# Performance work log

Measured on AMD Instinct MI355X. Metric: run time of the kernel, lower is better.

## Reference

```python
import jax, jax.numpy as jnp
import numpy as np

N_NODES = 50000
N_EDGES = 800000
D = 64
K_ORDER = 8


def setup_inputs() -> dict:
    key = jax.random.key(0)
    k1, k2, k3, k4 = jax.random.split(key, 4)
    x = jax.random.normal(k1, (N_NODES, D), dtype=jnp.float32)
    edge_index = jax.random.randint(k2, (2, N_EDGES), 0, N_NODES, dtype=jnp.int64)
    edge_weight = jax.random.uniform(k3, (N_EDGES,), dtype=jnp.float32)
    weight = jax.random.normal(k4, (K_ORDER, D, D), dtype=jnp.float32) * 0.05
    bias = jnp.zeros((D,), dtype=jnp.float32)
    return {"x": x, "edge_index": edge_index, "edge_weight": edge_weight,
            "weight": weight, "bias": bias}


def _propagate(h, src, dst, edge_weight, n_nodes):
    # sparse matvec: out[i] = sum_{e: dst_e = i} w_e * h[src_e]
    msgs = edge_weight[:, None] * h[src]          # (E, D)
    return jax.ops.segment_sum(msgs, dst, num_segments=n_nodes)


def reference(x, edge_index, edge_weight, weight, bias):
    src, dst = edge_index[0], edge_index[1]
    n = x.shape[0]
    K = weight.shape[0]
    # Chebyshev recursion: T_0 = x, T_1 = L x, T_k = 2 L T_{k-1} - T_{k-2}
    Tx_prev = x                                   # T_0
    out = jnp.einsum('nd,de->ne', Tx_prev, weight[0])
    Tx_cur = _propagate(x, src, dst, edge_weight, n)  # T_1
    if K > 1:
        out = out + jnp.einsum('nd,de->ne', Tx_cur, weight[1])
    for k in range(2, K):
        Tx_next = 2.0 * _propagate(Tx_cur, src, dst, edge_weight, n) - Tx_prev
        out = out + jnp.einsum('nd,de->ne', Tx_next, weight[k])
        Tx_prev, Tx_cur = Tx_cur, Tx_next
    return out + bias
```

## Files before the change

kernel.cpp:

```cpp
#include <hip/hip_runtime.h>
#include <hip/hip_fp16.h>

#define DD  64
#define BKT 256
#define CAP 4608
#define CHK 4096


__device__ __forceinline__ unsigned pk_bf16(float a, float b) {
    unsigned ua = __float_as_uint(a), ub = __float_as_uint(b);
    ua = (ua + 0x7fffu + ((ua >> 16) & 1u)) >> 16;
    ub = (ub + 0x7fffu + ((ub >> 16) & 1u)) & 0xffff0000u;
    return (ua & 0xffffu) | ub;
}
__device__ __forceinline__ void unpk_bf16(unsigned u, float& lo, float& hi) {
    lo = __uint_as_float(u << 16);
    hi = __uint_as_float(u & 0xffff0000u);
}


__global__ __launch_bounds__(256) void p1hist_kernel(
    const int* __restrict__ ei, int* __restrict__ bh, int E, int NB)
{
    __shared__ int lh[256];
    lh[threadIdx.x] = 0;
    __syncthreads();
    for (int e = blockIdx.x * 256 + threadIdx.x; e < E; e += gridDim.x * 256)
        atomicAdd(&lh[ei[E + e] >> 8], 1);
    __syncthreads();
    if (threadIdx.x < NB && lh[threadIdx.x])
        atomicAdd(&bh[threadIdx.x], lh[threadIdx.x]);
}

__global__ __launch_bounds__(256) void p1scan_kernel(
    const int* __restrict__ bh, int* __restrict__ bptr, int* __restrict__ bcur,
    int NB, int E)
{
    __shared__ int s[256];
    int t = threadIdx.x;
    int v = (t < NB) ? bh[t] : 0;
    s[t] = v;
    __syncthreads();
    for (int off = 1; off < 256; off <<= 1) {
        int u = (t >= off) ? s[t - off] : 0;
        __syncthreads();
        s[t] += u;
        __syncthreads();
    }
    if (t < NB) { int ex = s[t] - v; bptr[t] = ex; bcur[t] = ex; }
    if (t == 0) bptr[NB] = E;
}

__global__ __launch_bounds__(256) void p1fill_kernel(
    const int* __restrict__ ei, const float* __restrict__ ew,
    int* __restrict__ bcur, uint2* __restrict__ tmp, int E, int NB)
{
    __shared__ int lh[256], gb[256], lc[256];
    int tid = threadIdx.x;
    lh[tid] = 0;
    __syncthreads();
    int base = blockIdx.x * CHK;
#pragma unroll
    for (int j = 0; j < CHK / 256; ++j) {
        int e = base + j * 256 + tid;
        if (e < E) atomicAdd(&lh[ei[E + e] >> 8], 1);
    }
    __syncthreads();
    if (tid < NB) {
        gb[tid] = lh[tid] ? atomicAdd(&bcur[tid], lh[tid]) : 0;
        lc[tid] = 0;
    }
    __syncthreads();
#pragma unroll
    for (int j = 0; j < CHK / 256; ++j) {
        int e = base + j * 256 + tid;
        if (e < E) {
            int src = ei[e], dst = ei[E + e];
            unsigned short hw = __half_as_ushort(__float2half(ew[e]));
            unsigned rec = (unsigned)(unsigned short)src | ((unsigned)hw << 16);
            int b = dst >> 8;
            int pos = gb[b] + atomicAdd(&lc[b], 1);
            tmp[pos] = make_uint2(rec, (unsigned)(dst & 255));
        }
    }
}

__global__ __launch_bounds__(1024) void p2sort_kernel(
    const uint2* __restrict__ tmp, const int* __restrict__ bptr,
    unsigned* __restrict__ edges, int* __restrict__ row_ptr,
    int N, int E, int NB)
{
    __shared__ int lh[BKT], lx[BKT], lc[BKT];
    __shared__ unsigned lout[CAP];
    int b = blockIdx.x;
    int base = bptr[b];
    int cnt = bptr[b + 1] - base;
    if (cnt > CAP) cnt = CAP;
    int t = threadIdx.x;
    if (t < BKT) lh[t] = 0;
    __syncthreads();
    for (int i = t; i < cnt; i += 1024)
        atomicAdd(&lh[tmp[base + i].y & 255], 1);
    __syncthreads();
    if (t < BKT) { lc[t] = lh[t]; lx[t] = lh[t]; }
    __syncthreads();
    for (int off = 1; off < BKT; off <<= 1) {
        int v = 0;
        if (t < BKT && t >= off) v = lx[t - off];
        __syncthreads();
        if (t < BKT && t >= off) lx[t] += v;
        __syncthreads();
    }
    if (t < BKT) { lx[t] -= lc[t]; lc[t] = 0; }
    __syncthreads();
    for (int i = t; i < cnt; i += 1024) {
        uint2 r = tmp[base + i];
        int dl = r.y & 255;
        int pos = lx[dl] + atomicAdd(&lc[dl], 1);
        lout[pos] = r.x;
    }
    __syncthreads();
    for (int i = t; i < cnt; i += 1024) edges[base + i] = lout[i];
    if (t < BKT) {
        int d = b * BKT + t;
        if (d < N) row_ptr[d] = base + lx[t];
    }
    if (b == NB - 1 && t == 0) row_ptr[N] = E;
}

__global__ __launch_bounds__(256) void quant_kernel(
    const float4* __restrict__ src, uint4* __restrict__ dst, int n8)
{
    int i = blockIdx.x * 256 + threadIdx.x;
    if (i >= n8) return;
    float4 a = src[2 * i], b = src[2 * i + 1];
    dst[i] = make_uint4(pk_bf16(a.x, a.y), pk_bf16(a.z, a.w),
                        pk_bf16(b.x, b.y), pk_bf16(b.z, b.w));
}

__global__ __launch_bounds__(256) void prop_kernel(
    const unsigned short* __restrict__ h, const unsigned short* __restrict__ prev,
    const unsigned* __restrict__ edges, const int* __restrict__ row_ptr,
    unsigned short* __restrict__ Tnext, int N)
{
    int lane = threadIdx.x & 63;
    int wid  = (blockIdx.x * 256 + threadIdx.x) >> 6;
    int n0 = wid * 2, n1 = n0 + 1;
    if (n0 >= N) return;
    bool v1 = n1 < N;

    int g  = lane >> 3;
    int c8 = (lane & 7) << 3;

    int beg0 = row_ptr[n0];
    int end0 = row_ptr[n0 + 1];
    int beg1 = end0;
    int end1 = v1 ? row_ptr[n1 + 1] : end0;

    float4 A0 = make_float4(0.f, 0.f, 0.f, 0.f), A1 = A0;
    float4 B0 = A0, B1 = A0;

    int b0 = beg0, b1 = beg1;
    while (b0 < end0 || b1 < end1) {
        unsigned RA0 = (b0 + g     < end0) ? edges[b0 + g]     : 0u;
        unsigned RB0 = (b0 + 8 + g < end0) ? edges[b0 + 8 + g] : 0u;
        unsigned RA1 = (b1 + g     < end1) ? edges[b1 + g]     : 0u;
        unsigned RB1 = (b1 + 8 + g < end1) ? edges[b1 + 8 + g] : 0u;
        float wa0 = __half2float(__ushort_as_half((unsigned short)(RA0 >> 16)));
        float wb0 = __half2float(__ushort_as_half((unsigned short)(RB0 >> 16)));
        float wa1 = __half2float(__ushort_as_half((unsigned short)(RA1 >> 16)));
        float wb1 = __half2float(__ushort_as_half((unsigned short)(RB1 >> 16)));
        const uint4 va0 = *reinterpret_cast<const uint4*>(
            &h[(size_t)(RA0 & 0xffffu) * DD + c8]);
        const uint4 vb0 = *reinterpret_cast<const uint4*>(
            &h[(size_t)(RB0 & 0xffffu) * DD + c8]);
        const uint4 va1 = *reinterpret_cast<const uint4*>(
            &h[(size_t)(RA1 & 0xffffu) * DD + c8]);
        const uint4 vb1 = *reinterpret_cast<const uint4*>(
            &h[(size_t)(RB1 & 0xffffu) * DD + c8]);
        float lo, hi;
        unpk_bf16(va0.x, lo, hi); A0.x = fmaf(wa0, lo, A0.x); A0.y = fmaf(wa0, hi, A0.y);
        unpk_bf16(va0.y, lo, hi); A0.z = fmaf(wa0, lo, A0.z); A0.w = fmaf(wa0, hi, A0.w);
        unpk_bf16(va0.z, lo, hi); A1.x = fmaf(wa0, lo, A1.x); A1.y = fmaf(wa0, hi, A1.y);
        unpk_bf16(va0.w, lo, hi); A1.z = fmaf(wa0, lo, A1.z); A1.w = fmaf(wa0, hi, A1.w);
        unpk_bf16(vb0.x, lo, hi); A0.x = fmaf(wb0, lo, A0.x); A0.y = fmaf(wb0, hi, A0.y);
        unpk_bf16(vb0.y, lo, hi); A0.z = fmaf(wb0, lo, A0.z); A0.w = fmaf(wb0, hi, A0.w);
        unpk_bf16(vb0.z, lo, hi); A1.x = fmaf(wb0, lo, A1.x); A1.y = fmaf(wb0, hi, A1.y);
        unpk_bf16(vb0.w, lo, hi); A1.z = fmaf(wb0, lo, A1.z); A1.w = fmaf(wb0, hi, A1.w);
        unpk_bf16(va1.x, lo, hi); B0.x = fmaf(wa1, lo, B0.x); B0.y = fmaf(wa1, hi, B0.y);
        unpk_bf16(va1.y, lo, hi); B0.z = fmaf(wa1, lo, B0.z); B0.w = fmaf(wa1, hi, B0.w);
        unpk_bf16(va1.z, lo, hi); B1.x = fmaf(wa1, lo, B1.x); B1.y = fmaf(wa1, hi, B1.y);
        unpk_bf16(va1.w, lo, hi); B1.z = fmaf(wa1, lo, B1.z); B1.w = fmaf(wa1, hi, B1.w);
        unpk_bf16(vb1.x, lo, hi); B0.x = fmaf(wb1, lo, B0.x); B0.y = fmaf(wb1, hi, B0.y);
        unpk_bf16(vb1.y, lo, hi); B0.z = fmaf(wb1, lo, B0.z); B0.w = fmaf(wb1, hi, B0.w);
        unpk_bf16(vb1.z, lo, hi); B1.x = fmaf(wb1, lo, B1.x); B1.y = fmaf(wb1, hi, B1.y);
        unpk_bf16(vb1.w, lo, hi); B1.z = fmaf(wb1, lo, B1.z); B1.w = fmaf(wb1, hi, B1.w);
        b0 += 16; b1 += 16;
    }

#pragma unroll
    for (int mk = 8; mk <= 32; mk <<= 1) {
        A0.x += __shfl_xor(A0.x, mk); A0.y += __shfl_xor(A0.y, mk);
        A0.z += __shfl_xor(A0.z, mk); A0.w += __shfl_xor(A0.w, mk);
        A1.x += __shfl_xor(A1.x, mk); A1.y += __shfl_xor(A1.y, mk);
        A1.z += __shfl_xor(A1.z, mk); A1.w += __shfl_xor(A1.w, mk);
        B0.x += __shfl_xor(B0.x, mk); B0.y += __shfl_xor(B0.y, mk);
        B0.z += __shfl_xor(B0.z, mk); B0.w += __shfl_xor(B0.w, mk);
        B1.x += __shfl_xor(B1.x, mk); B1.y += __shfl_xor(B1.y, mk);
        B1.z += __shfl_xor(B1.z, mk); B1.w += __shfl_xor(B1.w, mk);
    }

    if (prev) {
        {
            const uint4 p = *reinterpret_cast<const uint4*>(&prev[(size_t)n0 * DD + c8]);
            float lo, hi;
            unpk_bf16(p.x, lo, hi); A0.x = 2.f * A0.x - lo; A0.y = 2.f * A0.y - hi;
            unpk_bf16(p.y, lo, hi); A0.z = 2.f * A0.z - lo; A0.w = 2.f * A0.w - hi;
            unpk_bf16(p.z, lo, hi); A1.x = 2.f * A1.x - lo; A1.y = 2.f * A1.y - hi;
            unpk_bf16(p.w, lo, hi); A1.z = 2.f * A1.z - lo; A1.w = 2.f * A1.w - hi;
        }
        if (v1) {
            const uint4 p = *reinterpret_cast<const uint4*>(&prev[(size_t)n1 * DD + c8]);
            float lo, hi;
            unpk_bf16(p.x, lo, hi); B0.x = 2.f * B0.x - lo; B0.y = 2.f * B0.y - hi;
            unpk_bf16(p.y, lo, hi); B0.z = 2.f * B0.z - lo; B0.w = 2.f * B0.w - hi;
            unpk_bf16(p.z, lo, hi); B1.x = 2.f * B1.x - lo; B1.y = 2.f * B1.y - hi;
            unpk_bf16(p.w, lo, hi); B1.z = 2.f * B1.z - lo; B1.w = 2.f * B1.w - hi;
        }
    }
    if (g == 0) {
        *reinterpret_cast<uint4*>(&Tnext[(size_t)n0 * DD + c8]) =
            make_uint4(pk_bf16(A0.x, A0.y), pk_bf16(A0.z, A0.w),
                       pk_bf16(A1.x, A1.y), pk_bf16(A1.z, A1.w));
        if (v1)
            *reinterpret_cast<uint4*>(&Tnext[(size_t)n1 * DD + c8]) =
                make_uint4(pk_bf16(B0.x, B0.y), pk_bf16(B0.z, B0.w),
                           pk_bf16(B1.x, B1.y), pk_bf16(B1.z, B1.w));
    }
}

__global__ __launch_bounds__(512) void mega_gemm_kernel(
    const unsigned short* __restrict__ T0, const unsigned short* __restrict__ T1,
    const unsigned short* __restrict__ T2, const unsigned short* __restrict__ T3,
    const float* __restrict__ W, const float* __restrict__ bias,
    float* __restrict__ out, int N, int nord, int init)
{
    __shared__ float Ws[DD * DD];
    __shared__ float Ts[64][68];
    const unsigned short* Tl[4] = { T0, T1, T2, T3 };

    int nb0 = blockIdx.x * 64;
    int r = threadIdx.x >> 4, c = threadIdx.x & 15;
    int r2 = r * 2, c4 = c * 4;

    float acc[2][4];
    if (init) {
        const float4 bb = *reinterpret_cast<const float4*>(&bias[c4]);
#pragma unroll
        for (int i = 0; i < 2; ++i) {
            acc[i][0] = bb.x; acc[i][1] = bb.y; acc[i][2] = bb.z; acc[i][3] = bb.w;
        }
    } else {
#pragma unroll
        for (int i = 0; i < 2; ++i)
            acc[i][0] = acc[i][1] = acc[i][2] = acc[i][3] = 0.f;
    }

    int nl = threadIdx.x & 63, q = threadIdx.x >> 6;
    for (int kc = 0; kc < nord; ++kc) {
        __syncthreads();
        for (int i = threadIdx.x; i < DD * DD; i += 512)
            Ws[i] = W[kc * DD * DD + i];
        {
            uint4 u = make_uint4(0, 0, 0, 0);
            if (nb0 + nl < N)
                u = *reinterpret_cast<const uint4*>(
                    &Tl[kc][(size_t)(nb0 + nl) * DD + q * 8]);
            float f0, f1, f2, f3, f4, f5, f6, f7;
            unpk_bf16(u.x, f0, f1); unpk_bf16(u.y, f2, f3);
            unpk_bf16(u.z, f4, f5); unpk_bf16(u.w, f6, f7);
            *reinterpret_cast<float4*>(&Ts[nl][q * 8])     = make_float4(f0, f1, f2, f3);
            *reinterpret_cast<float4*>(&Ts[nl][q * 8 + 4]) = make_float4(f4, f5, f6, f7);
        }
        __syncthreads();
#pragma unroll 8
        for (int d = 0; d < DD; ++d) {
            float a0 = Ts[r2 + 0][d], a1 = Ts[r2 + 1][d];
            float4 b = *reinterpret_cast<const float4*>(&Ws[d * DD + c4]);
            acc[0][0] = fmaf(a0, b.x, acc[0][0]); acc[0][1] = fmaf(a0, b.y, acc[0][1]);
            acc[0][2] = fmaf(a0, b.z, acc[0][2]); acc[0][3] = fmaf(a0, b.w, acc[0][3]);
            acc[1][0] = fmaf(a1, b.x, acc[1][0]); acc[1][1] = fmaf(a1, b.y, acc[1][1]);
            acc[1][2] = fmaf(a1, b.z, acc[1][2]); acc[1][3] = fmaf(a1, b.w, acc[1][3]);
        }
    }

#pragma unroll
    for (int i = 0; i < 2; ++i) {
        int n = nb0 + r2 + i;
        if (n < N) {
            float4 o = make_float4(acc[i][0], acc[i][1], acc[i][2], acc[i][3]);
            if (!init) {
                float4 p = *reinterpret_cast<const float4*>(&out[(size_t)n * DD + c4]);
                o.x += p.x; o.y += p.y; o.z += p.z; o.w += p.w;
            }
            *reinterpret_cast<float4*>(&out[(size_t)n * DD + c4]) = o;
        }
    }
}


static inline size_t rup(size_t x) { return (x + 255) & ~(size_t)255; }

extern "C" void kernel_launch(void* const* d_in, const int* in_sizes, int n_in,
                              void* d_out, int out_size, void* d_ws, size_t ws_size,
                              hipStream_t stream) {
    const float* x    = (const float*)d_in[0];
    const int*   ei   = (const int*)  d_in[1];
    const float* ew   = (const float*)d_in[2];
    const float* W    = (const float*)d_in[3];
    const float* bias = (const float*)d_in[4];
    float* out = (float*)d_out;

    int N = in_sizes[0] / DD;
    int E = in_sizes[2];
    int K = in_sizes[3] / (DD * DD);
    int NB = (N + BKT - 1) / BKT;

    size_t nb_bf = (size_t)N * DD * sizeof(unsigned short);

    char* w = (char*)d_ws;
    unsigned short* B[5];
    for (int i = 0; i < 5; ++i) { B[i] = (unsigned short*)w; w += rup(nb_bf); }
    unsigned* edges  = (unsigned*)w;  w += rup((size_t)E * sizeof(unsigned));
    int* row_ptr = (int*)w;           w += rup((size_t)(N + 1) * sizeof(int));
    int* bh      = (int*)w;           w += rup((size_t)NB * sizeof(int));
    int* bptr    = (int*)w;           w += rup((size_t)(NB + 1) * sizeof(int));
    int* bcur    = (int*)w;           w += rup((size_t)NB * sizeof(int));
    uint2* tmp   = (uint2*)B[1];

    int pb   = (N + 7) / 8;
    int gb64 = (N + 63) / 64;
    int n8   = (N * DD) / 8;
    int qb   = (n8 + 255) / 256;
    int fb   = (E + CHK - 1) / CHK;

    hipMemsetAsync(bh, 0, (size_t)NB * sizeof(int), stream);
    p1hist_kernel<<<512, 256, 0, stream>>>(ei, bh, E, NB);
    p1scan_kernel<<<1, 256, 0, stream>>>(bh, bptr, bcur, NB, E);
    p1fill_kernel<<<fb, 256, 0, stream>>>(ei, ew, bcur, tmp, E, NB);
    p2sort_kernel<<<NB, 1024, 0, stream>>>(tmp, bptr, edges, row_ptr, N, E, NB);

    quant_kernel<<<qb, 256, 0, stream>>>((const float4*)x, (uint4*)B[0], n8);

    int done = 0;
    for (int k = 1; k < K; ++k) {
        const unsigned short* cur  = B[(k - 1) % 5];
        const unsigned short* prev = (k >= 2) ? B[(k - 2) % 5] : nullptr;
        unsigned short*       nxt  = B[k % 5];
        prop_kernel<<<pb, 256, 0, stream>>>(cur, prev, edges, row_ptr, nxt, N);
        if (k % 4 == 3) {
            int c0 = done;
            mega_gemm_kernel<<<gb64, 512, 0, stream>>>(
                B[(c0 + 0) % 5], B[(c0 + 1) % 5], B[(c0 + 2) % 5], B[(c0 + 3) % 5],
                W + (size_t)c0 * DD * DD, bias, out, N, 4, done == 0);
            done += 4;
        }
    }
    if (done < K) {
        mega_gemm_kernel<<<gb64, 512, 0, stream>>>(
            B[(done + 0) % 5], B[(done + 1) % 5],
            B[(done + 2) % 5], B[(done + 3) % 5],
            W + (size_t)done * DD * DD, bias, out, N, K - done, done == 0);
    }
}
```

Baseline: 266.0 us.

## Prefetch next-order T and W into registers in GEMM; halve block tile

```diff
diff --git a/kernel.cpp b/kernel.cpp
--- a/kernel.cpp
+++ b/kernel.cpp
@@ -239,18 +239,19 @@
     }
 }
 
-__global__ __launch_bounds__(512) void mega_gemm_kernel(
+__global__ __launch_bounds__(256) void mega_gemm_kernel(
     const unsigned short* __restrict__ T0, const unsigned short* __restrict__ T1,
     const unsigned short* __restrict__ T2, const unsigned short* __restrict__ T3,
     const float* __restrict__ W, const float* __restrict__ bias,
     float* __restrict__ out, int N, int nord, int init)
 {
     __shared__ float Ws[DD * DD];
-    __shared__ float Ts[64][68];
+    __shared__ float Ts[32][68];
     const unsigned short* Tl[4] = { T0, T1, T2, T3 };
 
-    int nb0 = blockIdx.x * 64;
-    int r = threadIdx.x >> 4, c = threadIdx.x & 15;
+    int nb0 = blockIdx.x * 32;
+    int tid = threadIdx.x;
+    int r = tid >> 4, c = tid & 15;
     int r2 = r * 2, c4 = c * 4;
 
     float acc[2][4];
@@ -266,23 +267,38 @@
             acc[i][0] = acc[i][1] = acc[i][2] = acc[i][3] = 0.f;
     }
 
-    int nl = threadIdx.x & 63, q = threadIdx.x >> 6;
+    int nl = tid >> 3, q = tid & 7;
+    bool tvalid = (nb0 + nl) < N;
+
+    uint4 tv = make_uint4(0, 0, 0, 0);
+    float wv[16];
+    if (tvalid)
+        tv = *reinterpret_cast<const uint4*>(&Tl[0][(size_t)(nb0 + nl) * DD + q * 8]);
+#pragma unroll
+    for (int j = 0; j < 16; ++j) wv[j] = W[tid + j * 256];
+
     for (int kc = 0; kc < nord; ++kc) {
         __syncthreads();
-        for (int i = threadIdx.x; i < DD * DD; i += 512)
-            Ws[i] = W[kc * DD * DD + i];
         {
-            uint4 u = make_uint4(0, 0, 0, 0);
-            if (nb0 + nl < N)
-                u = *reinterpret_cast<const uint4*>(
-                    &Tl[kc][(size_t)(nb0 + nl) * DD + q * 8]);
             float f0, f1, f2, f3, f4, f5, f6, f7;
-            unpk_bf16(u.x, f0, f1); unpk_bf16(u.y, f2, f3);
-            unpk_bf16(u.z, f4, f5); unpk_bf16(u.w, f6, f7);
+            unpk_bf16(tv.x, f0, f1); unpk_bf16(tv.y, f2, f3);
+            unpk_bf16(tv.z, f4, f5); unpk_bf16(tv.w, f6, f7);
             *reinterpret_cast<float4*>(&Ts[nl][q * 8])     = make_float4(f0, f1, f2, f3);
             *reinterpret_cast<float4*>(&Ts[nl][q * 8 + 4]) = make_float4(f4, f5, f6, f7);
-        }
-        __syncthreads();
+#pragma unroll
+            for (int j = 0; j < 16; ++j) Ws[tid + j * 256] = wv[j];
+        }
+        __syncthreads();
+
+        if (kc + 1 < nord) {
+            if (tvalid)
+                tv = *reinterpret_cast<const uint4*>(
+                    &Tl[kc + 1][(size_t)(nb0 + nl) * DD + q * 8]);
+            const float* Wn = W + (size_t)(kc + 1) * DD * DD;
+#pragma unroll
+            for (int j = 0; j < 16; ++j) wv[j] = Wn[tid + j * 256];
+        }
+
 #pragma unroll 8
         for (int d = 0; d < DD; ++d) {
             float a0 = Ts[r2 + 0][d], a1 = Ts[r2 + 1][d];
@@ -339,7 +355,7 @@
     uint2* tmp   = (uint2*)B[1];
 
     int pb   = (N + 7) / 8;
-    int gb64 = (N + 63) / 64;
+    int gb32 = (N + 31) / 32;
     int n8   = (N * DD) / 8;
     int qb   = (n8 + 255) / 256;
     int fb   = (E + CHK - 1) / CHK;
@@ -360,14 +376,14 @@
         prop_kernel<<<pb, 256, 0, stream>>>(cur, prev, edges, row_ptr, nxt, N);
         if (k % 4 == 3) {
             int c0 = done;
-            mega_gemm_kernel<<<gb64, 512, 0, stream>>>(
+            mega_gemm_kernel<<<gb32, 256, 0, stream>>>(
                 B[(c0 + 0) % 5], B[(c0 + 1) % 5], B[(c0 + 2) % 5], B[(c0 + 3) % 5],
                 W + (size_t)c0 * DD * DD, bias, out, N, 4, done == 0);
             done += 4;
         }
     }
     if (done < K) {
-        mega_gemm_kernel<<<gb64, 512, 0, stream>>>(
+        mega_gemm_kernel<<<gb32, 256, 0, stream>>>(
             B[(done + 0) % 5], B[(done + 1) % 5],
             B[(done + 2) % 5], B[(done + 3) % 5],
             W + (size_t)done * DD * DD, bias, out, N, K - done, done == 0);
```

Measured after the change: 259.3 us. -2.5%, faster.
